# Kernel optimization log

Hardware: AMD Instinct MI355X
Metric: run time of the kernel (lower is better)

The kernel has to match this reference:

```python
import jax, jax.numpy as jnp
import numpy as np
from jax import lax

B, T = 256, 512
D_DEC, D_ENC2, D_ATT = 512, 1024, 128
N_FILT, K = 32, 31
PAD = (K - 1) // 2


def setup_inputs() -> dict:
    key = jax.random.key(0)
    ks = jax.random.split(key, 10)
    s = 0.02
    return {
        "query": jax.random.normal(ks[0], (B, D_DEC), jnp.float32),
        "encoder_output": jax.random.normal(ks[1], (B, T, D_ENC2), jnp.float32),
        "attention_weights": jax.random.uniform(ks[2], (B, T), jnp.float32),
        "Wq": jax.random.normal(ks[3], (D_DEC, D_ATT), jnp.float32) * s,
        "Wk": jax.random.normal(ks[4], (D_ENC2, D_ATT), jnp.float32) * s,
        "Wv": jax.random.normal(ks[5], (D_ENC2, D_DEC), jnp.float32) * s,
        "Wloc": jax.random.normal(ks[6], (N_FILT, D_ATT), jnp.float32) * s,
        "conv_w": jax.random.normal(ks[7], (N_FILT, 1, K), jnp.float32) * s,
        "conv_b": jax.random.normal(ks[8], (N_FILT,), jnp.float32) * s,
        "Wscore": jax.random.normal(ks[9], (D_ATT, 1), jnp.float32) * s,
    }


def reference(query, encoder_output, attention_weights, Wq, Wk, Wv, Wloc, conv_w, conv_b, Wscore):
    # query projection: (B, D_att), broadcast over time
    q = (query @ Wq)[:, None, :]                      # (B, 1, D_att)
    k = encoder_output @ Wk                           # (B, T, D_att)
    # location features: conv1d over previous attention weights
    loc = lax.conv_general_dilated(
        attention_weights[:, None, :],                # (B, 1, T)
        conv_w,                                       # (F, 1, K)
        window_strides=(1,),
        padding=[(PAD, PAD)],
        dimension_numbers=("NCH", "OIH", "NCH"),
    ) + conv_b[None, :, None]                         # (B, F, T)
    loc = jnp.einsum("bft,fa->bta", loc, Wloc)        # (B, T, D_att)
    energy = jnp.tanh(q + k + loc) @ Wscore           # (B, T, 1)
    new_w = jax.nn.softmax(energy[..., 0], axis=1)    # (B, T)
    context = jnp.einsum("bt,btd->bd", new_w, encoder_output) @ Wv  # (B, D_dec)
    return context, new_w
```

## Files before the change

### kernel.cpp

```cpp
#include <hip/hip_runtime.h>
#include <hip/hip_bf16.h>

typedef __attribute__((ext_vector_type(8))) short bf16x8;
typedef __attribute__((ext_vector_type(4))) float f32x4;

#define NB   256
#define TT   512
#define DDEC 512
#define DENC 1024
#define DATT 128
#define NF   32
#define KW   31
#define PW   15

struct SMem {
  union {
    struct {
      __hip_bfloat16 locA[512][40];
      __hip_bfloat16 locBt[128][40];
    } l;
    float part[16][1024];
  } u;
  float qpart[8][128];
  float attw[TT];
  float qrow[DDEC];
  float cw[NF][32];
  float cb[NF];
  float qv[DATT];
  float wsc[DATT];
  float energy[TT];
  float red[16];
  float scal[2];
};

__device__ __forceinline__ float fast_tanh(float x) {
  float e = __expf(2.f * x);
  return 1.f - 2.f / (e + 1.f);
}

__global__ __launch_bounds__(256) void prep_wkt(const float* __restrict__ Wk,
                                                __hip_bfloat16* __restrict__ WkT) {
  int idx = blockIdx.x * 256 + threadIdx.x;
  int k2 = idx >> 7, a = idx & 127;
  int k = k2 * 2;
  union { ushort2 u; __hip_bfloat16 h[2]; } cv;
  cv.h[0] = __float2bfloat16(Wk[(size_t)k * DATT + a]);
  cv.h[1] = __float2bfloat16(Wk[(size_t)(k + 1) * DATT + a]);
  *reinterpret_cast<ushort2*>(WkT + (size_t)a * 1024 + k) = cv.u;
}

__global__ __launch_bounds__(1024) void pass1_kernel(
    const float* __restrict__ query,
    const float* __restrict__ enc,
    const float* __restrict__ attw,
    const float* __restrict__ Wq,
    const __hip_bfloat16* __restrict__ WkT,
    const float* __restrict__ Wloc,
    const float* __restrict__ convw,
    const float* __restrict__ convb,
    const float* __restrict__ wscore,
    float* __restrict__ out_w,
    float* __restrict__ ctx_enc) {
  __shared__ SMem sm;
  const int b    = blockIdx.x;
  const int tid  = threadIdx.x;
  const int lane = tid & 63;
  const int wv   = tid >> 6;
  const int lrow = lane & 15;
  const int lgrp = lane >> 4;

  if (tid < TT) {
    sm.attw[tid] = attw[(size_t)b * TT + tid];
    sm.qrow[tid] = query[(size_t)b * DDEC + tid];
  }
  if (tid < NF * KW) sm.cw[tid / KW][tid % KW] = convw[tid];
  if (tid < NF)   sm.cb[tid]  = convb[tid];
  if (tid < DATT) sm.wsc[tid] = wscore[tid];
  for (int i = tid; i < NF * DATT; i += 1024) {
    int f = i >> 7, a = i & 127;
    sm.u.l.locBt[a][f] = __float2bfloat16(Wloc[i]);
  }
  __syncthreads();

  {
    const int p = tid >> 7, a = tid & 127;
    float acc = 0.f;
    const float* wq = Wq + (size_t)(p * 64) * DATT + a;
#pragma unroll 8
    for (int d = 0; d < 64; ++d)
      acc = fmaf(sm.qrow[p * 64 + d], wq[(size_t)d * DATT], acc);
    sm.qpart[p][a] = acc;
  }
  {
    const int t = tid & 511, h = tid >> 9;
#pragma unroll
    for (int f0 = 0; f0 < 16; ++f0) {
      const int f = h * 16 + f0;
      float acc = sm.cb[f];
      for (int k = 0; k < KW; ++k) {
        int ts = t - PW + k;
        float x = (ts >= 0 && ts < TT) ? sm.attw[ts] : 0.f;
        acc = fmaf(sm.cw[f][k], x, acc);
      }
      sm.u.l.locA[t][f] = __float2bfloat16(acc);
    }
  }
  __syncthreads();
  if (tid < DATT) {
    float s = 0.f;
#pragma unroll
    for (int p = 0; p < 8; ++p) s += sm.qpart[p][tid];
    sm.qv[tid] = s;
  }

  f32x4 acc[2][8];
  {
    bf16x8 af[2], bfr[8];
#pragma unroll
    for (int m = 0; m < 2; ++m)
      af[m] = *reinterpret_cast<const bf16x8*>(
          &sm.u.l.locA[wv * 32 + m * 16 + lrow][lgrp * 8]);
#pragma unroll
    for (int n = 0; n < 8; ++n)
      bfr[n] = *reinterpret_cast<const bf16x8*>(
          &sm.u.l.locBt[n * 16 + lrow][lgrp * 8]);
#pragma unroll
    for (int m = 0; m < 2; ++m)
#pragma unroll
      for (int n = 0; n < 8; ++n)
        acc[m][n] = __builtin_amdgcn_mfma_f32_16x16x32_bf16(
            af[m], bfr[n], (f32x4){0.f, 0.f, 0.f, 0.f}, 0, 0, 0);
  }
  __syncthreads();

  const float* pa0 = enc + (((size_t)b * TT) + wv * 32 + lrow) * DENC + lgrp * 8;
  const __hip_bfloat16* pb = WkT + lrow * 1024 + lgrp * 8;

  for (int c = 0; c < 16; ++c) {
    const int k0 = c * 64;
#pragma unroll
    for (int s = 0; s < 2; ++s) {
      const int ko = k0 + s * 32;
      bf16x8 af[2];
#pragma unroll
      for (int m = 0; m < 2; ++m) {
        const float* p = pa0 + (size_t)m * 16 * DENC + ko;
        float4 v0 = *reinterpret_cast<const float4*>(p);
        float4 v1 = *reinterpret_cast<const float4*>(p + 4);
        union { bf16x8 v; __hip_bfloat16 h[8]; } cv;
        cv.h[0] = __float2bfloat16(v0.x); cv.h[1] = __float2bfloat16(v0.y);
        cv.h[2] = __float2bfloat16(v0.z); cv.h[3] = __float2bfloat16(v0.w);
        cv.h[4] = __float2bfloat16(v1.x); cv.h[5] = __float2bfloat16(v1.y);
        cv.h[6] = __float2bfloat16(v1.z); cv.h[7] = __float2bfloat16(v1.w);
        af[m] = cv.v;
      }
      bf16x8 bfr[8];
#pragma unroll
      for (int n = 0; n < 8; ++n)
        bfr[n] = *reinterpret_cast<const bf16x8*>(pb + (size_t)n * 16 * 1024 + ko);
#pragma unroll
      for (int m = 0; m < 2; ++m)
#pragma unroll
        for (int n = 0; n < 8; ++n)
          acc[m][n] = __builtin_amdgcn_mfma_f32_16x16x32_bf16(
              af[m], bfr[n], acc[m][n], 0, 0, 0);
    }
  }

#pragma unroll
  for (int m = 0; m < 2; ++m) {
#pragma unroll
    for (int r = 0; r < 4; ++r) {
      float e = 0.f;
#pragma unroll
      for (int n = 0; n < 8; ++n) {
        int col = n * 16 + lrow;
        float v = acc[m][n][r] + sm.qv[col];
        e = fmaf(fast_tanh(v), sm.wsc[col], e);
      }
      e += __shfl_xor(e, 1);
      e += __shfl_xor(e, 2);
      e += __shfl_xor(e, 4);
      e += __shfl_xor(e, 8);
      if (lrow == 0) sm.energy[wv * 32 + m * 16 + lgrp * 4 + r] = e;
    }
  }
  __syncthreads();

  const float e0 = (tid < TT) ? sm.energy[tid] : -1e30f;
  float m1 = e0;
#pragma unroll
  for (int off = 1; off < 64; off <<= 1) m1 = fmaxf(m1, __shfl_xor(m1, off));
  if (lane == 0) sm.red[wv] = m1;
  __syncthreads();
  if (tid == 0) {
    float mm = sm.red[0];
#pragma unroll
    for (int i = 1; i < 16; ++i) mm = fmaxf(mm, sm.red[i]);
    sm.scal[0] = mm;
  }
  __syncthreads();
  const float ex = (tid < TT) ? __expf(e0 - sm.scal[0]) : 0.f;
  float s1 = ex;
#pragma unroll
  for (int off = 1; off < 64; off <<= 1) s1 += __shfl_xor(s1, off);
  if (lane == 0) sm.red[wv] = s1;
  __syncthreads();
  if (tid == 0) {
    float ss = 0.f;
#pragma unroll
    for (int i = 0; i < 16; ++i) ss += sm.red[i];
    sm.scal[1] = 1.f / ss;
  }
  __syncthreads();
  if (tid < TT) {
    const float wnorm = ex * sm.scal[1];
    sm.energy[tid] = wnorm;
    out_w[(size_t)b * TT + tid] = wnorm;
  }
  __syncthreads();

  float4 a0 = {0,0,0,0}, a1 = {0,0,0,0}, a2 = {0,0,0,0}, a3 = {0,0,0,0};
  const int t0 = wv * 32;
  for (int tt = 0; tt < 32; ++tt) {
    const int t = t0 + tt;
    const float wt = sm.energy[t];
    const float4* row =
        reinterpret_cast<const float4*>(enc + ((size_t)b * TT + t) * DENC);
    float4 v0 = row[lane];
    float4 v1 = row[64 + lane];
    float4 v2 = row[128 + lane];
    float4 v3 = row[192 + lane];
    a0.x = fmaf(wt, v0.x, a0.x); a0.y = fmaf(wt, v0.y, a0.y);
    a0.z = fmaf(wt, v0.z, a0.z); a0.w = fmaf(wt, v0.w, a0.w);
    a1.x = fmaf(wt, v1.x, a1.x); a1.y = fmaf(wt, v1.y, a1.y);
    a1.z = fmaf(wt, v1.z, a1.z); a1.w = fmaf(wt, v1.w, a1.w);
    a2.x = fmaf(wt, v2.x, a2.x); a2.y = fmaf(wt, v2.y, a2.y);
    a2.z = fmaf(wt, v2.z, a2.z); a2.w = fmaf(wt, v2.w, a2.w);
    a3.x = fmaf(wt, v3.x, a3.x); a3.y = fmaf(wt, v3.y, a3.y);
    a3.z = fmaf(wt, v3.z, a3.z); a3.w = fmaf(wt, v3.w, a3.w);
  }
  *reinterpret_cast<float4*>(&sm.u.part[wv][lane * 4])       = a0;
  *reinterpret_cast<float4*>(&sm.u.part[wv][256 + lane * 4]) = a1;
  *reinterpret_cast<float4*>(&sm.u.part[wv][512 + lane * 4]) = a2;
  *reinterpret_cast<float4*>(&sm.u.part[wv][768 + lane * 4]) = a3;
  __syncthreads();
  {
    const int d = tid;
    float s = 0.f;
#pragma unroll
    for (int w = 0; w < 16; ++w) s += sm.u.part[w][d];
    ctx_enc[(size_t)b * DENC + d] = s;
  }
}

__global__ __launch_bounds__(512) void ctx_proj_kernel(
    const float* __restrict__ ctx_enc,
    const float* __restrict__ Wv,
    float* __restrict__ out) {
  __shared__ float sc[DENC];
  const int b = blockIdx.x, tid = threadIdx.x;
  for (int i = tid; i < DENC; i += 512) sc[i] = ctx_enc[(size_t)b * DENC + i];
  __syncthreads();
  float acc = 0.f;
#pragma unroll 8
  for (int d = 0; d < DENC; ++d)
    acc = fmaf(sc[d], Wv[(size_t)d * DDEC + tid], acc);
  out[(size_t)b * DDEC + tid] = acc;
}

extern "C" void kernel_launch(void* const* d_in, const int* in_sizes, int n_in,
                              void* d_out, int out_size, void* d_ws, size_t ws_size,
                              hipStream_t stream) {
  const float* query  = (const float*)d_in[0];
  const float* enc    = (const float*)d_in[1];
  const float* attw   = (const float*)d_in[2];
  const float* Wq     = (const float*)d_in[3];
  const float* Wk     = (const float*)d_in[4];
  const float* Wv     = (const float*)d_in[5];
  const float* Wloc   = (const float*)d_in[6];
  const float* convw  = (const float*)d_in[7];
  const float* convb  = (const float*)d_in[8];
  const float* wscore = (const float*)d_in[9];

  float* ctx     = (float*)d_out;
  float* neww    = (float*)d_out + NB * TT;
  float* ctx_enc = (float*)d_ws;
  __hip_bfloat16* WkT =
      (__hip_bfloat16*)((char*)d_ws + (size_t)NB * DENC * sizeof(float));

  hipLaunchKernelGGL(prep_wkt, dim3(256), dim3(256), 0, stream, Wk, WkT);
  hipLaunchKernelGGL(pass1_kernel, dim3(NB), dim3(1024), 0, stream,
                     query, enc, attw, Wq, WkT, Wloc, convw, convb, wscore,
                     neww, ctx_enc);
  hipLaunchKernelGGL(ctx_proj_kernel, dim3(NB), dim3(512), 0, stream,
                     ctx_enc, Wv, ctx);
}
```

Baseline: 390.9 us.

## Split fused attention kernel into energy, softmax and context kernels with async LDS pipelining

```diff
diff --git a/kernel.cpp b/kernel.cpp
--- a/kernel.cpp
+++ b/kernel.cpp
@@ -13,25 +13,10 @@
 #define KW   31
 #define PW   15
 
-struct SMem {
-  union {
-    struct {
-      __hip_bfloat16 locA[512][40];
-      __hip_bfloat16 locBt[128][40];
-    } l;
-    float part[16][1024];
-  } u;
-  float qpart[8][128];
-  float attw[TT];
-  float qrow[DDEC];
-  float cw[NF][32];
-  float cb[NF];
-  float qv[DATT];
-  float wsc[DATT];
-  float energy[TT];
-  float red[16];
-  float scal[2];
-};
+#define GLDS16(g, l)                                                        \
+  __builtin_amdgcn_global_load_lds(                                         \
+      (const __attribute__((address_space(1))) void*)(uintptr_t)(g),        \
+      (__attribute__((address_space(3))) void*)(uintptr_t)(l), 16, 0, 0)
 
 __device__ __forceinline__ float fast_tanh(float x) {
   float e = __expf(2.f * x);
@@ -49,223 +34,243 @@
   *reinterpret_cast<ushort2*>(WkT + (size_t)a * 1024 + k) = cv.u;
 }
 
-__global__ __launch_bounds__(1024) void pass1_kernel(
-    const float* __restrict__ query,
+__global__ __launch_bounds__(128) void prep_qv(const float* __restrict__ query,
+                                               const float* __restrict__ Wq,
+                                               float* __restrict__ qvg) {
+  __shared__ float qr[DDEC];
+  const int b = blockIdx.x, tid = threadIdx.x;
+  for (int i = tid; i < DDEC; i += 128) qr[i] = query[(size_t)b * DDEC + i];
+  __syncthreads();
+  float a0 = 0.f, a1 = 0.f, a2 = 0.f, a3 = 0.f;
+#pragma unroll 4
+  for (int d = 0; d < DDEC; d += 4) {
+    a0 = fmaf(qr[d + 0], Wq[(size_t)(d + 0) * DATT + tid], a0);
+    a1 = fmaf(qr[d + 1], Wq[(size_t)(d + 1) * DATT + tid], a1);
+    a2 = fmaf(qr[d + 2], Wq[(size_t)(d + 2) * DATT + tid], a2);
+    a3 = fmaf(qr[d + 3], Wq[(size_t)(d + 3) * DATT + tid], a3);
+  }
+  qvg[(size_t)b * DATT + tid] = (a0 + a1) + (a2 + a3);
+}
+
+struct K1SMem {
+  float astage[8][2][16][32];
+  __hip_bfloat16 locA[8][16][32];
+  __hip_bfloat16 locBt[128][32];
+  float attw_loc[160];
+  float qv[DATT];
+  float wsc[DATT];
+};
+
+__global__ __launch_bounds__(512, 6) void energy_kernel(
     const float* __restrict__ enc,
-    const float* __restrict__ attw,
-    const float* __restrict__ Wq,
+    const float* __restrict__ attwg,
     const __hip_bfloat16* __restrict__ WkT,
+    const float* __restrict__ qvg,
     const float* __restrict__ Wloc,
     const float* __restrict__ convw,
     const float* __restrict__ convb,
     const float* __restrict__ wscore,
-    float* __restrict__ out_w,
-    float* __restrict__ ctx_enc) {
-  __shared__ SMem sm;
-  const int b    = blockIdx.x;
-  const int tid  = threadIdx.x;
-  const int lane = tid & 63;
-  const int wv   = tid >> 6;
-  const int lrow = lane & 15;
-  const int lgrp = lane >> 4;
-
-  if (tid < TT) {
-    sm.attw[tid] = attw[(size_t)b * TT + tid];
-    sm.qrow[tid] = query[(size_t)b * DDEC + tid];
-  }
-  if (tid < NF * KW) sm.cw[tid / KW][tid % KW] = convw[tid];
-  if (tid < NF)   sm.cb[tid]  = convb[tid];
-  if (tid < DATT) sm.wsc[tid] = wscore[tid];
-  for (int i = tid; i < NF * DATT; i += 1024) {
+    float* __restrict__ energy_ws) {
+  __shared__ K1SMem sm;
+  const int b = blockIdx.x >> 2, q = blockIdx.x & 3;
+  const int tid = threadIdx.x;
+  const int lane = tid & 63, wv = tid >> 6;
+  const int lrow = lane & 15, lgrp = lane >> 4;
+
+  if (tid < DATT) {
+    sm.qv[tid] = qvg[(size_t)b * DATT + tid];
+    sm.wsc[tid] = wscore[tid];
+  }
+  if (tid < 160) {
+    int g = q * 128 - PW + tid;
+    sm.attw_loc[tid] = (g >= 0 && g < TT) ? attwg[(size_t)b * TT + g] : 0.f;
+  }
+  for (int i = tid; i < NF * DATT; i += 512) {
     int f = i >> 7, a = i & 127;
-    sm.u.l.locBt[a][f] = __float2bfloat16(Wloc[i]);
-  }
-  __syncthreads();
-
+    sm.locBt[a][f] = __float2bfloat16(Wloc[i]);
+  }
+  __syncthreads();
+
+  const int f = lane & 31;
+  float cwreg[KW];
+#pragma unroll
+  for (int k = 0; k < KW; ++k) cwreg[k] = convw[f * KW + k];
+  const float cbreg = convb[f];
+
+  const float* gsrc_base =
+      enc + ((size_t)b * TT + q * 128 + wv * 16 + (lane >> 3)) * DENC +
+      (((lane & 7) ^ (lane >> 3)) << 2);
+  const __hip_bfloat16* pb = WkT + (size_t)lrow * 1024 + lgrp * 8;
+
+  bf16x8 barrA[8], barrB[8];
   {
-    const int p = tid >> 7, a = tid & 127;
-    float acc = 0.f;
-    const float* wq = Wq + (size_t)(p * 64) * DATT + a;
-#pragma unroll 8
-    for (int d = 0; d < 64; ++d)
-      acc = fmaf(sm.qrow[p * 64 + d], wq[(size_t)d * DATT], acc);
-    sm.qpart[p][a] = acc;
-  }
+    char* d0 = (char*)&sm.astage[wv][0][0][0];
+    GLDS16(gsrc_base, d0);
+    GLDS16(gsrc_base + (size_t)8 * DENC, d0 + 1024);
+#pragma unroll
+    for (int n = 0; n < 8; ++n)
+      barrA[n] = *reinterpret_cast<const bf16x8*>(pb + (size_t)n * 16384);
+  }
+
   {
-    const int t = tid & 511, h = tid >> 9;
-#pragma unroll
-    for (int f0 = 0; f0 < 16; ++f0) {
-      const int f = h * 16 + f0;
-      float acc = sm.cb[f];
-      for (int k = 0; k < KW; ++k) {
-        int ts = t - PW + k;
-        float x = (ts >= 0 && ts < TT) ? sm.attw[ts] : 0.f;
-        acc = fmaf(sm.cw[f][k], x, acc);
-      }
-      sm.u.l.locA[t][f] = __float2bfloat16(acc);
+    float att[38];
+    const int rbase = (lane >> 5) * 8;
+#pragma unroll
+    for (int i = 0; i < 38; ++i) att[i] = sm.attw_loc[wv * 16 + rbase + i];
+#pragma unroll
+    for (int rr = 0; rr < 8; ++rr) {
+      float acc = cbreg;
+#pragma unroll
+      for (int k = 0; k < KW; ++k) acc = fmaf(cwreg[k], att[rr + k], acc);
+      sm.locA[wv][rbase + rr][f] = __float2bfloat16(acc);
     }
   }
-  __syncthreads();
-  if (tid < DATT) {
-    float s = 0.f;
-#pragma unroll
-    for (int p = 0; p < 8; ++p) s += sm.qpart[p][tid];
-    sm.qv[tid] = s;
-  }
-
-  f32x4 acc[2][8];
+
+  f32x4 acc[8];
   {
-    bf16x8 af[2], bfr[8];
-#pragma unroll
-    for (int m = 0; m < 2; ++m)
-      af[m] = *reinterpret_cast<const bf16x8*>(
-          &sm.u.l.locA[wv * 32 + m * 16 + lrow][lgrp * 8]);
-#pragma unroll
-    for (int n = 0; n < 8; ++n)
-      bfr[n] = *reinterpret_cast<const bf16x8*>(
-          &sm.u.l.locBt[n * 16 + lrow][lgrp * 8]);
-#pragma unroll
-    for (int m = 0; m < 2; ++m)
-#pragma unroll
-      for (int n = 0; n < 8; ++n)
-        acc[m][n] = __builtin_amdgcn_mfma_f32_16x16x32_bf16(
-            af[m], bfr[n], (f32x4){0.f, 0.f, 0.f, 0.f}, 0, 0, 0);
-  }
-  __syncthreads();
-
-  const float* pa0 = enc + (((size_t)b * TT) + wv * 32 + lrow) * DENC + lgrp * 8;
-  const __hip_bfloat16* pb = WkT + lrow * 1024 + lgrp * 8;
-
-  for (int c = 0; c < 16; ++c) {
-    const int k0 = c * 64;
-#pragma unroll
-    for (int s = 0; s < 2; ++s) {
-      const int ko = k0 + s * 32;
-      bf16x8 af[2];
-#pragma unroll
-      for (int m = 0; m < 2; ++m) {
-        const float* p = pa0 + (size_t)m * 16 * DENC + ko;
-        float4 v0 = *reinterpret_cast<const float4*>(p);
-        float4 v1 = *reinterpret_cast<const float4*>(p + 4);
-        union { bf16x8 v; __hip_bfloat16 h[8]; } cv;
-        cv.h[0] = __float2bfloat16(v0.x); cv.h[1] = __float2bfloat16(v0.y);
-        cv.h[2] = __float2bfloat16(v0.z); cv.h[3] = __float2bfloat16(v0.w);
-        cv.h[4] = __float2bfloat16(v1.x); cv.h[5] = __float2bfloat16(v1.y);
-        cv.h[6] = __float2bfloat16(v1.z); cv.h[7] = __float2bfloat16(v1.w);
-        af[m] = cv.v;
-      }
-      bf16x8 bfr[8];
-#pragma unroll
-      for (int n = 0; n < 8; ++n)
-        bfr[n] = *reinterpret_cast<const bf16x8*>(pb + (size_t)n * 16 * 1024 + ko);
-#pragma unroll
-      for (int m = 0; m < 2; ++m)
-#pragma unroll
-        for (int n = 0; n < 8; ++n)
-          acc[m][n] = __builtin_amdgcn_mfma_f32_16x16x32_bf16(
-              af[m], bfr[n], acc[m][n], 0, 0, 0);
+    bf16x8 af = *reinterpret_cast<const bf16x8*>(&sm.locA[wv][lrow][lgrp * 8]);
+#pragma unroll
+    for (int n = 0; n < 8; ++n) {
+      bf16x8 bl = *reinterpret_cast<const bf16x8*>(&sm.locBt[n * 16 + lrow][lgrp * 8]);
+      acc[n] = __builtin_amdgcn_mfma_f32_16x16x32_bf16(
+          af, bl, (f32x4){0.f, 0.f, 0.f, 0.f}, 0, 0, 0);
     }
   }
 
-#pragma unroll
-  for (int m = 0; m < 2; ++m) {
-#pragma unroll
-    for (int r = 0; r < 4; ++r) {
-      float e = 0.f;
-#pragma unroll
-      for (int n = 0; n < 8; ++n) {
-        int col = n * 16 + lrow;
-        float v = acc[m][n][r] + sm.qv[col];
-        e = fmaf(fast_tanh(v), sm.wsc[col], e);
-      }
-      e += __shfl_xor(e, 1);
-      e += __shfl_xor(e, 2);
-      e += __shfl_xor(e, 4);
-      e += __shfl_xor(e, 8);
-      if (lrow == 0) sm.energy[wv * 32 + m * 16 + lgrp * 4 + r] = e;
+#define K1_STEP(BUFSEL, BNOW, BNEXT, TILE)                                    \
+  {                                                                           \
+    if ((TILE) + 1 < 32) {                                                    \
+      const int nt_ = (TILE) + 1;                                             \
+      char* d0_ = (char*)&sm.astage[wv][(BUFSEL) ^ 1][0][0];                  \
+      GLDS16(gsrc_base + nt_ * 32, d0_);                                      \
+      GLDS16(gsrc_base + nt_ * 32 + (size_t)8 * DENC, d0_ + 1024);            \
+      _Pragma("unroll")                                                       \
+      for (int n = 0; n < 8; ++n)                                             \
+        BNEXT[n] = *reinterpret_cast<const bf16x8*>(                          \
+            pb + (size_t)n * 16384 + nt_ * 32);                               \
+      __builtin_amdgcn_sched_barrier(0);                                      \
+      asm volatile("s_waitcnt vmcnt(10)" ::: "memory");                       \
+      __builtin_amdgcn_sched_barrier(0);                                      \
+    } else {                                                                  \
+      __builtin_amdgcn_sched_barrier(0);                                      \
+      asm volatile("s_waitcnt vmcnt(0)" ::: "memory");                        \
+      __builtin_amdgcn_sched_barrier(0);                                      \
+    }                                                                         \
+    const char* rb_ = (const char*)&sm.astage[wv][(BUFSEL)][0][0];            \
+    const int x_ = lrow & 7;                                                  \
+    float4 f0_ = *reinterpret_cast<const float4*>(                            \
+        rb_ + lrow * 128 + (((2 * lgrp) ^ x_) << 4));                         \
+    float4 f1_ = *reinterpret_cast<const float4*>(                            \
+        rb_ + lrow * 128 + (((2 * lgrp + 1) ^ x_) << 4));                     \
+    union { bf16x8 v; __hip_bfloat16 h[8]; } cv_;                             \
+    cv_.h[0] = __float2bfloat16(f0_.x); cv_.h[1] = __float2bfloat16(f0_.y);   \
+    cv_.h[2] = __float2bfloat16(f0_.z); cv_.h[3] = __float2bfloat16(f0_.w);   \
+    cv_.h[4] = __float2bfloat16(f1_.x); cv_.h[5] = __float2bfloat16(f1_.y);   \
+    cv_.h[6] = __float2bfloat16(f1_.z); cv_.h[7] = __float2bfloat16(f1_.w);   \
+    _Pragma("unroll")                                                         \
+    for (int n = 0; n < 8; ++n)                                               \
+      acc[n] = __builtin_amdgcn_mfma_f32_16x16x32_bf16(                       \
+          cv_.v, BNOW[n], acc[n], 0, 0, 0);                                   \
+  }
+
+#pragma unroll 1
+  for (int c = 0; c < 32; c += 2) {
+    K1_STEP(0, barrA, barrB, c)
+    K1_STEP(1, barrB, barrA, c + 1)
+  }
+#undef K1_STEP
+
+#pragma unroll
+  for (int r = 0; r < 4; ++r) {
+    float e = 0.f;
+#pragma unroll
+    for (int n = 0; n < 8; ++n) {
+      const int col = n * 16 + lrow;
+      float v = acc[n][r] + sm.qv[col];
+      e = fmaf(fast_tanh(v), sm.wsc[col], e);
     }
-  }
-  __syncthreads();
-
-  const float e0 = (tid < TT) ? sm.energy[tid] : -1e30f;
+    e += __shfl_xor(e, 1);
+    e += __shfl_xor(e, 2);
+    e += __shfl_xor(e, 4);
+    e += __shfl_xor(e, 8);
+    if (lrow == 0)
+      energy_ws[(size_t)b * TT + q * 128 + wv * 16 + lgrp * 4 + r] = e;
+  }
+}
+
+__global__ __launch_bounds__(512) void softmax_kernel(
+    const float* __restrict__ energy_ws, float* __restrict__ out_w) {
+  __shared__ float red[8];
+  __shared__ float scal[2];
+  const int b = blockIdx.x, tid = threadIdx.x;
+  const int lane = tid & 63, wv = tid >> 6;
+  const float e0 = energy_ws[(size_t)b * TT + tid];
   float m1 = e0;
 #pragma unroll
   for (int off = 1; off < 64; off <<= 1) m1 = fmaxf(m1, __shfl_xor(m1, off));
-  if (lane == 0) sm.red[wv] = m1;
+  if (lane == 0) red[wv] = m1;
   __syncthreads();
   if (tid == 0) {
-    float mm = sm.red[0];
-#pragma unroll
-    for (int i = 1; i < 16; ++i) mm = fmaxf(mm, sm.red[i]);
-    sm.scal[0] = mm;
-  }
-  __syncthreads();
-  const float ex = (tid < TT) ? __expf(e0 - sm.scal[0]) : 0.f;
+    float mm = red[0];
+#pragma unroll
+    for (int i = 1; i < 8; ++i) mm = fmaxf(mm, red[i]);
+    scal[0] = mm;
+  }
+  __syncthreads();
+  const float ex = __expf(e0 - scal[0]);
   float s1 = ex;
 #pragma unroll
   for (int off = 1; off < 64; off <<= 1) s1 += __shfl_xor(s1, off);
-  if (lane == 0) sm.red[wv] = s1;
+  if (lane == 0) red[wv] = s1;
   __syncthreads();
   if (tid == 0) {
     float ss = 0.f;
 #pragma unroll
-    for (int i = 0; i < 16; ++i) ss += sm.red[i];
-    sm.scal[1] = 1.f / ss;
-  }
-  __syncthreads();
-  if (tid < TT) {
-    const float wnorm = ex * sm.scal[1];
-    sm.energy[tid] = wnorm;
-    out_w[(size_t)b * TT + tid] = wnorm;
-  }
-  __syncthreads();
-
-  float4 a0 = {0,0,0,0}, a1 = {0,0,0,0}, a2 = {0,0,0,0}, a3 = {0,0,0,0};
-  const int t0 = wv * 32;
-  for (int tt = 0; tt < 32; ++tt) {
-    const int t = t0 + tt;
-    const float wt = sm.energy[t];
-    const float4* row =
-        reinterpret_cast<const float4*>(enc + ((size_t)b * TT + t) * DENC);
-    float4 v0 = row[lane];
-    float4 v1 = row[64 + lane];
-    float4 v2 = row[128 + lane];
-    float4 v3 = row[192 + lane];
-    a0.x = fmaf(wt, v0.x, a0.x); a0.y = fmaf(wt, v0.y, a0.y);
-    a0.z = fmaf(wt, v0.z, a0.z); a0.w = fmaf(wt, v0.w, a0.w);
-    a1.x = fmaf(wt, v1.x, a1.x); a1.y = fmaf(wt, v1.y, a1.y);
-    a1.z = fmaf(wt, v1.z, a1.z); a1.w = fmaf(wt, v1.w, a1.w);
-    a2.x = fmaf(wt, v2.x, a2.x); a2.y = fmaf(wt, v2.y, a2.y);
-    a2.z = fmaf(wt, v2.z, a2.z); a2.w = fmaf(wt, v2.w, a2.w);
-    a3.x = fmaf(wt, v3.x, a3.x); a3.y = fmaf(wt, v3.y, a3.y);
-    a3.z = fmaf(wt, v3.z, a3.z); a3.w = fmaf(wt, v3.w, a3.w);
-  }
-  *reinterpret_cast<float4*>(&sm.u.part[wv][lane * 4])       = a0;
-  *reinterpret_cast<float4*>(&sm.u.part[wv][256 + lane * 4]) = a1;
-  *reinterpret_cast<float4*>(&sm.u.part[wv][512 + lane * 4]) = a2;
-  *reinterpret_cast<float4*>(&sm.u.part[wv][768 + lane * 4]) = a3;
-  __syncthreads();
-  {
-    const int d = tid;
-    float s = 0.f;
-#pragma unroll
-    for (int w = 0; w < 16; ++w) s += sm.u.part[w][d];
-    ctx_enc[(size_t)b * DENC + d] = s;
-  }
+    for (int i = 0; i < 8; ++i) ss += red[i];
+    scal[1] = 1.f / ss;
+  }
+  __syncthreads();
+  out_w[(size_t)b * TT + tid] = ex * scal[1];
+}
+
+__global__ __launch_bounds__(256) void ctx_partial_kernel(
+    const float* __restrict__ enc, const float* __restrict__ w,
+    float* __restrict__ ctxp) {
+  __shared__ float ws[128];
+  const int b = blockIdx.x >> 2, q = blockIdx.x & 3;
+  const int tid = threadIdx.x;
+  if (tid < 128) ws[tid] = w[(size_t)b * TT + q * 128 + tid];
+  __syncthreads();
+  const float* base = enc + ((size_t)b * TT + q * 128) * DENC + tid * 4;
+  float4 a = {0.f, 0.f, 0.f, 0.f};
+#pragma unroll 8
+  for (int r = 0; r < 128; ++r) {
+    float4 v = *reinterpret_cast<const float4*>(base + (size_t)r * DENC);
+    const float wt = ws[r];
+    a.x = fmaf(wt, v.x, a.x);
+    a.y = fmaf(wt, v.y, a.y);
+    a.z = fmaf(wt, v.z, a.z);
+    a.w = fmaf(wt, v.w, a.w);
+  }
+  *reinterpret_cast<float4*>(ctxp + ((size_t)(b * 4 + q)) * DENC + tid * 4) = a;
 }
 
 __global__ __launch_bounds__(512) void ctx_proj_kernel(
-    const float* __restrict__ ctx_enc,
-    const float* __restrict__ Wv,
+    const float* __restrict__ ctxp, const float* __restrict__ Wv,
     float* __restrict__ out) {
   __shared__ float sc[DENC];
   const int b = blockIdx.x, tid = threadIdx.x;
-  for (int i = tid; i < DENC; i += 512) sc[i] = ctx_enc[(size_t)b * DENC + i];
+  for (int i = tid; i < DENC; i += 512) {
+    float s = 0.f;
+#pragma unroll
+    for (int qq = 0; qq < 4; ++qq) s += ctxp[((size_t)(b * 4 + qq)) * DENC + i];
+    sc[i] = s;
+  }
   __syncthreads();
   float acc = 0.f;
 #pragma unroll 8
-  for (int d = 0; d < DENC; ++d)
-    acc = fmaf(sc[d], Wv[(size_t)d * DDEC + tid], acc);
+  for (int dd = 0; dd < DENC; ++dd)
+    acc = fmaf(sc[dd], Wv[(size_t)dd * DDEC + tid], acc);
   out[(size_t)b * DDEC + tid] = acc;
 }
 
@@ -283,16 +288,23 @@
   const float* convb  = (const float*)d_in[8];
   const float* wscore = (const float*)d_in[9];
 
-  float* ctx     = (float*)d_out;
-  float* neww    = (float*)d_out + NB * TT;
-  float* ctx_enc = (float*)d_ws;
-  __hip_bfloat16* WkT =
-      (__hip_bfloat16*)((char*)d_ws + (size_t)NB * DENC * sizeof(float));
+  float* ctx  = (float*)d_out;
+  float* neww = (float*)d_out + NB * TT;
+
+  char* ws = (char*)d_ws;
+  float* ctxp      = (float*)ws;
+  __hip_bfloat16* WkT = (__hip_bfloat16*)(ws + 4194304);
+  float* qvg       = (float*)(ws + 4194304 + 262144);
+  float* energy_ws = (float*)(ws + 4194304 + 262144 + 131072);
 
   hipLaunchKernelGGL(prep_wkt, dim3(256), dim3(256), 0, stream, Wk, WkT);
-  hipLaunchKernelGGL(pass1_kernel, dim3(NB), dim3(1024), 0, stream,
-                     query, enc, attw, Wq, WkT, Wloc, convw, convb, wscore,
-                     neww, ctx_enc);
+  hipLaunchKernelGGL(prep_qv, dim3(NB), dim3(128), 0, stream, query, Wq, qvg);
+  hipLaunchKernelGGL(energy_kernel, dim3(NB * 4), dim3(512), 0, stream,
+                     enc, attw, WkT, qvg, Wloc, convw, convb, wscore, energy_ws);
+  hipLaunchKernelGGL(softmax_kernel, dim3(NB), dim3(512), 0, stream,
+                     energy_ws, neww);
+  hipLaunchKernelGGL(ctx_partial_kernel, dim3(NB * 4), dim3(256), 0, stream,
+                     enc, neww, ctxp);
   hipLaunchKernelGGL(ctx_proj_kernel, dim3(NB), dim3(512), 0, stream,
-                     ctx_enc, Wv, ctx);
-}
+                     ctxp, Wv, ctx);
+}
```

Result: slower. 922.6 us (+136.0%).
